# Optimization experiments

Measured on AMD Instinct MI355X. Metric: run time of the kernel, lower is better.

The kernel has to match this reference:

```python
import jax, jax.numpy as jnp
import numpy as np

EPS = 1e-06


def _create_circular_masks(h, w):
    # Faithful to the torch code: y spans width, x spans height -> mask shape (w, h).
    # Only used with square feature maps (h == w), matching the module's implicit assumption.
    cen_w, cen_h = w // 2, h // 2
    y = np.arange(-cen_w, w - cen_w).reshape(-1, 1)
    x = np.arange(-cen_h, h - cen_h).reshape(1, -1)
    y2, x2 = y * y, x * x
    r2 = x2 + y2
    masks = [r2 <= 0]
    max_r = int(np.sqrt(r2.max())) + 1
    quadrants = [(1, 1), (-1, 1), (1, -1), (-1, -1)]  # (sign_x, sign_y)
    for radius in range(1, max_r):
        lo, hi = (radius - 1) ** 2, radius ** 2
        for sx, sy in quadrants:
            quad = (sx * x >= 0) & (sy * y >= 0)
            masks.append((r2 > lo) & (r2 <= hi) & quad)  # ring mask
            masks.append((r2 <= hi) & quad)              # circle mask
    return np.stack(masks).astype(np.float32)  # [M, w, h] == [M, h, w] for square maps


def _l2_normalize(v):
    # v: [B, C]; torch norms over dim=1 with eps added to the norm
    return v / (jnp.linalg.norm(v, axis=1, keepdims=True) + EPS)


def setup_inputs() -> dict:
    key = jax.random.key(0)
    x = jax.random.normal(key, (32, 1024, 28, 28), dtype=jnp.float32)
    return {"x": x}


def reference(x) -> jnp.ndarray:
    B, C, H, W = x.shape
    masks = jnp.asarray(_create_circular_masks(H, W))  # [M, H, W] static constant
    # Global descriptor: max-pool over full map, then channel-wise L2 normalize.
    v = _l2_normalize(jnp.max(x, axis=(2, 3)))  # [B, C]
    # Accumulate masked-max descriptors; scan over the (fixed) mask set keeps
    # peak memory at one masked feature map instead of M of them.
    def step(acc, mask):
        vt = jnp.max(x * mask, axis=(2, 3))  # masked max-pool (zeros included, as in torch)
        return acc + _l2_normalize(vt), None
    v, _ = jax.lax.scan(step, v, masks)
    return v[:, :, None, None]  # [B, C, 1, 1] to match F.max_pool2d output shape
```

## Files before the change

kernel.cpp:

```cpp
#include <hip/hip_runtime.h>
#include <math.h>

#define B_DIM 32
#define C_DIM 1024
#define MAP 784
#define NMASK 153
#define NTERM 154
#define NROW 160
#define NBIN 77
#define DUMMY_BIN 77
#define MAX1 28
#define MAX2 6
#define MPW 8
#define NBLK 1024
#define GRP 32

struct Sched {
    unsigned short off1[MAX1][64];
    unsigned short off2[MAX2][64];
    unsigned char  binA[64];
    unsigned char  binB[64];
    bool ok;
};

constexpr Sched build_sched() {
    Sched S{};
    S.ok = true;
    short px[NBIN][40] = {};
    int   n[NBIN] = {};
    for (int i = 0; i < 28; ++i)
        for (int j = 0; j < 28; ++j) {
            int dy = i - 14, dx = j - 14, r2 = dx * dx + dy * dy;
            int p = i * 28 + j;
            if (r2 == 0) { px[0][n[0]++] = (short)p; continue; }
            if (r2 > 361) continue;
            int r = 0; while (r * r < r2) ++r;
            const int sx[4] = {1, -1, 1, -1}, sy[4] = {1, 1, -1, -1};
            for (int q = 0; q < 4; ++q)
                if (sx[q] * dx >= 0 && sy[q] * dy >= 0) {
                    int b = 1 + q * 19 + (r - 1);
                    if (n[b] >= 40) { S.ok = false; continue; }
                    px[b][n[b]++] = (short)p;
                }
        }
    int ord[NBIN] = {};
    for (int k = 0; k < NBIN; ++k) ord[k] = k;
    for (int a = 0; a < NBIN; ++a) {
        int best = a;
        for (int c = a + 1; c < NBIN; ++c)
            if (n[ord[c]] > n[ord[best]]) best = c;
        int t = ord[a]; ord[a] = ord[best]; ord[best] = t;
    }
    for (int l = 0; l < 64; ++l) {
        S.binA[l] = (unsigned char)ord[l];
        S.binB[l] = (l >= 51) ? (unsigned char)ord[64 + (l - 51)]
                              : (unsigned char)DUMMY_BIN;
        if (n[ord[l]] > MAX1) S.ok = false;
        if (l >= 51 && n[ord[64 + (l - 51)]] > MAX2) S.ok = false;
    }
    {
        bool used[64][40] = {};
        for (int s = 0; s < MAX1; ++s) {
            int bankcnt[32] = {};
            for (int l = 0; l < 64; ++l) {
                int bin = S.binA[l], cnt = n[bin];
                int bestp = 0, bestload = 1 << 30; bool haveUnused = false;
                for (int t = 0; t < cnt; ++t)
                    if (!used[l][t]) {
                        int load = bankcnt[px[bin][t] % 32];
                        if (!haveUnused || load < bestload) { haveUnused = true; bestload = load; bestp = t; }
                    }
                if (!haveUnused)
                    for (int t = 0; t < cnt; ++t) {
                        int load = bankcnt[px[bin][t] % 32];
                        if (load < bestload) { bestload = load; bestp = t; }
                    }
                int p = px[bin][bestp];
                if (haveUnused) used[l][bestp] = true;
                S.off1[s][l] = (unsigned short)(p * 4);
                bankcnt[p % 32]++;
            }
        }
        for (int l = 0; l < 64; ++l)
            for (int t = 0; t < n[S.binA[l]]; ++t)
                if (!used[l][t]) S.ok = false;
    }
    {
        bool used[64][40] = {};
        for (int s = 0; s < MAX2; ++s) {
            int bankcnt[32] = {};
            for (int l = 0; l < 64; ++l) {
                if (S.binB[l] == DUMMY_BIN) {
                    S.off2[s][l] = (unsigned short)((l % 32) * 4);
                    continue;
                }
                int bin = S.binB[l], cnt = n[bin];
                int bestp = 0, bestload = 1 << 30; bool haveUnused = false;
                for (int t = 0; t < cnt; ++t)
                    if (!used[l][t]) {
                        int load = bankcnt[px[bin][t] % 32];
                        if (!haveUnused || load < bestload) { haveUnused = true; bestload = load; bestp = t; }
                    }
                if (!haveUnused)
                    for (int t = 0; t < cnt; ++t) {
                        int load = bankcnt[px[bin][t] % 32];
                        if (load < bestload) { bestload = load; bestp = t; }
                    }
                int p = px[bin][bestp];
                if (haveUnused) used[l][bestp] = true;
                S.off2[s][l] = (unsigned short)(p * 4);
                bankcnt[p % 32]++;
            }
        }
        for (int l = 0; l < 64; ++l)
            if (S.binB[l] != DUMMY_BIN)
                for (int t = 0; t < n[S.binB[l]]; ++t)
                    if (!used[l][t]) S.ok = false;
    }
    return S;
}

static_assert(build_sched().ok, "schedule overflow / unplaced pixel");
__constant__ Sched d_sched = build_sched();

__device__ __forceinline__ int term_addr(int k) {
    if (k == 0) return 0;
    if (k >= NMASK) return DUMMY_BIN;
    int t = k - 1, q = (t >> 1) & 3, rm1 = t >> 3;
    return (t & 1) ? 78 + q * 19 + rm1
                   : 1 + q * 19 + rm1;
}

__global__ __launch_bounds__(256) void cac_fused(const float* __restrict__ x,
                                                 float* __restrict__ partial,
                                                 unsigned int* __restrict__ bar,
                                                 float* __restrict__ out) {
    __shared__ __align__(16) float smap[4][MAP];
    __shared__ float sbuf[4][160];
    __shared__ float ssqred[4][NROW];
    __shared__ float sinv[NROW];

    const int wave = threadIdx.x >> 6;
    const int lane = threadIdx.x & 63;
    const int map0 = blockIdx.x * (4 * MPW) + wave * MPW;

    const int linA = lane % 19;
    const bool inA = lane < 57, inB = lane < 19;
    const int rbA = 1 + lane;
    const int rbB = inB ? 58 + lane : DUMMY_BIN;
    const int a0 = term_addr(lane);
    const int a1 = term_addr(lane + 64);
    const int a2 = term_addr(lane + 128);

    const float4 NEG4 = make_float4(-INFINITY, -INFINITY, -INFINITY, -INFINITY);
    const float4* xp4 = (const float4*)(x + (size_t)map0 * MAP);
    float4 t0 = xp4[lane], t1 = xp4[64 + lane], t2 = xp4[128 + lane];
    float4 t3 = NEG4;
    if (lane < 4) t3 = xp4[192 + lane];

    float* smw = smap[wave];
    float* sbw = sbuf[wave];
    float sq0 = 0.0f, sq1 = 0.0f, sq2 = 0.0f;
    float rr0[MPW], rr1[MPW], rr2[MPW];

    #pragma unroll
    for (int m = 0; m < MPW; ++m) {
        ((float4*)smw)[lane]       = t0;
        ((float4*)smw)[64 + lane]  = t1;
        ((float4*)smw)[128 + lane] = t2;
        if (lane < 4) ((float4*)smw)[192 + lane] = t3;
        float gmax = fmaxf(fmaxf(fmaxf(t0.x, t0.y), fmaxf(t0.z, t0.w)),
                           fmaxf(fmaxf(t1.x, t1.y), fmaxf(t1.z, t1.w)));
        gmax = fmaxf(gmax, fmaxf(fmaxf(t2.x, t2.y), fmaxf(t2.z, t2.w)));
        gmax = fmaxf(gmax, fmaxf(fmaxf(t3.x, t3.y), fmaxf(t3.z, t3.w)));

        if (m < MPW - 1) {
            const float4* np4 = (const float4*)(x + (size_t)(map0 + m + 1) * MAP);
            t0 = np4[lane]; t1 = np4[64 + lane]; t2 = np4[128 + lane];
            t3 = NEG4;
            if (lane < 4) t3 = np4[192 + lane];
        }
        __builtin_amdgcn_wave_barrier();

        const char* base = (const char*)smw;
        float m1 = 0.0f, m2v = 0.0f;
        #pragma unroll
        for (int s = 0; s < MAX1; ++s)
            m1 = fmaxf(m1, *(const float*)(base + d_sched.off1[s][lane]));
        #pragma unroll
        for (int s = 0; s < MAX2; ++s)
            m2v = fmaxf(m2v, *(const float*)(base + d_sched.off2[s][lane]));
        sbw[d_sched.binA[lane]] = m1;
        sbw[d_sched.binB[lane]] = m2v;

        #pragma unroll
        for (int off = 32; off; off >>= 1)
            gmax = fmaxf(gmax, __shfl_xor(gmax, off, 64));
        __builtin_amdgcn_wave_barrier();

        float cval = sbw[0];
        float rA = fmaxf(sbw[rbA], cval);
        float rB = fmaxf(sbw[rbB], cval);
        #pragma unroll
        for (int s = 1; s <= 16; s <<= 1) {
            float uA = __shfl_up(rA, s, 64);
            float uB = __shfl_up(rB, s, 64);
            if (linA >= s) rA = fmaxf(rA, uA);
            if (lane >= s) rB = fmaxf(rB, uB);
        }
        if (inA) sbw[78 + lane] = rA;
        if (inB) sbw[135 + lane] = rB;
        __builtin_amdgcn_wave_barrier();

        float r0 = sbw[a0];
        float r1 = sbw[a1];
        float r2 = sbw[a2];
        r2 = (lane == 25) ? gmax : (lane < 26 ? r2 : 0.0f);

        rr0[m] = r0; rr1[m] = r1; rr2[m] = r2;
        sq0 += r0 * r0; sq1 += r1 * r1; sq2 += r2 * r2;
        __builtin_amdgcn_wave_barrier();
    }

    ssqred[wave][lane]      = sq0;
    ssqred[wave][64 + lane] = sq1;
    if (lane < 32) ssqred[wave][128 + lane] = sq2;
    __syncthreads();
    if (threadIdx.x < NROW) {
        int t = threadIdx.x;
        float v = ssqred[0][t] + ssqred[1][t] + ssqred[2][t] + ssqred[3][t];
        __hip_atomic_store(&partial[(size_t)blockIdx.x * NROW + t], v,
                           __ATOMIC_RELAXED, __HIP_MEMORY_SCOPE_AGENT);
    }
    __syncthreads();

    unsigned int* gbar = bar + (size_t)(blockIdx.x >> 5) * 64;
    if (threadIdx.x == 0) {
        __hip_atomic_fetch_add(gbar, 1u, __ATOMIC_RELAXED, __HIP_MEMORY_SCOPE_AGENT);
        int budget = 1 << 17;
        while (__hip_atomic_load(gbar, __ATOMIC_RELAXED, __HIP_MEMORY_SCOPE_AGENT) < GRP
               && --budget)
            __builtin_amdgcn_s_sleep(16);
    }
    __syncthreads();

    if (threadIdx.x < NROW) {
        int t = threadIdx.x;
        const float* p = partial + (size_t)(blockIdx.x & ~31) * NROW + t;
        float s = 0.0f;
        #pragma unroll 16
        for (int j = 0; j < GRP; ++j)
            s += __hip_atomic_load(&p[(size_t)j * NROW],
                                   __ATOMIC_RELAXED, __HIP_MEMORY_SCOPE_AGENT);
        sinv[t] = (t < NTERM) ? 1.0f / (sqrtf(s) + 1e-6f) : 0.0f;
    }
    __syncthreads();

    const float sl0 = sinv[lane];
    const float sl1 = sinv[64 + lane];
    const float sl2 = (lane < 32) ? sinv[128 + lane] : 0.0f;
    #pragma unroll
    for (int m = 0; m < MPW; ++m) {
        float acc = rr0[m] * sl0 + rr1[m] * sl1 + rr2[m] * sl2;
        #pragma unroll
        for (int off = 32; off; off >>= 1)
            acc += __shfl_xor(acc, off, 64);
        if (lane == 0) out[map0 + m] = acc;
    }
}

extern "C" void kernel_launch(void* const* d_in, const int* in_sizes, int n_in,
                              void* d_out, int out_size, void* d_ws, size_t ws_size,
                              hipStream_t stream) {
    const float* x = (const float*)d_in[0];
    float* out = (float*)d_out;

    float* partial = (float*)d_ws;
    unsigned int* bar = (unsigned int*)((char*)d_ws +
                          (size_t)NBLK * NROW * sizeof(float));

    hipMemsetAsync(bar, 0, 32 * 64 * sizeof(unsigned int), stream);
    cac_fused<<<NBLK, 256, 0, stream>>>(x, partial, bar, out);
}
```

Before: 157.9 us.

## Pair bins across lane pairs to balance per-lane gather work

Bins are now grouped into 32 load-balanced pairs, and each pair's pixels are split evenly over two adjacent lanes. Each lane tracks two partial maxima using per-step select bitmasks, and the pairs are combined with an xor shuffle. This cuts the longest per-lane LDS gather chain from 28 to 18 steps. In exchange each step does extra bitmask tests and selects, and every map adds a shuffle combine.

```diff
diff --git a/kernel.cpp b/kernel.cpp
--- a/kernel.cpp
+++ b/kernel.cpp
@@ -9,7 +9,7 @@
 #define NROW 160
 #define NBIN 77
 #define DUMMY_BIN 77
-#define MAX1 28
+#define MAX1 18
 #define MAX2 6
 #define MPW 8
 #define NBLK 1024
@@ -17,9 +17,11 @@
 
 struct Sched {
     unsigned short off1[MAX1][64];
+    unsigned long long selA[MAX1];
+    unsigned long long selB[MAX1];
     unsigned short off2[MAX2][64];
-    unsigned char  binA[64];
-    unsigned char  binB[64];
+    unsigned char binW[64];
+    unsigned char binB[64];
     bool ok;
 };
 
@@ -52,37 +54,77 @@
         int t = ord[a]; ord[a] = ord[best]; ord[best] = t;
     }
     for (int l = 0; l < 64; ++l) {
-        S.binA[l] = (unsigned char)ord[l];
         S.binB[l] = (l >= 51) ? (unsigned char)ord[64 + (l - 51)]
                               : (unsigned char)DUMMY_BIN;
-        if (n[ord[l]] > MAX1) S.ok = false;
         if (l >= 51 && n[ord[64 + (l - 51)]] > MAX2) S.ok = false;
     }
+
+    int pairBins[32][2] = {};
+    int pairCnt[32] = {};
+    int pairLoad[32] = {};
+    for (int i = 0; i < 64; ++i) {
+        int best = -1;
+        for (int p = 0; p < 32; ++p)
+            if (pairCnt[p] < 2 && (best < 0 || pairLoad[p] < pairLoad[best]))
+                best = p;
+        if (best < 0) { S.ok = false; best = 0; }
+        pairBins[best][pairCnt[best]] = ord[i];
+        pairCnt[best]++;
+        pairLoad[best] += n[ord[i]];
+    }
+
+    short ipix[64][40] = {};
+    signed char iflag[64][40] = {};
+    int icnt[64] = {};
+    for (int p = 0; p < 32; ++p) {
+        int bA = pairBins[p][0], bB = pairBins[p][1];
+        S.binW[2 * p]     = (unsigned char)bA;
+        S.binW[2 * p + 1] = (unsigned char)bB;
+        short cp[80] = {}; signed char cf[80] = {}; int cl = 0;
+        for (int t = 0; t < n[bA]; ++t) { cp[cl] = px[bA][t]; cf[cl] = 0; ++cl; }
+        for (int t = 0; t < n[bB]; ++t) { cp[cl] = px[bB][t]; cf[cl] = 1; ++cl; }
+        int h = (cl + 1) / 2;
+        if (h > MAX1 || (cl - h) > MAX1) S.ok = false;
+        for (int t = 0; t < h && t < 40; ++t) {
+            ipix[2 * p][icnt[2 * p]] = cp[t]; iflag[2 * p][icnt[2 * p]] = cf[t];
+            ++icnt[2 * p];
+        }
+        for (int t = h; t < cl && (t - h) < 40; ++t) {
+            ipix[2 * p + 1][icnt[2 * p + 1]] = cp[t];
+            iflag[2 * p + 1][icnt[2 * p + 1]] = cf[t];
+            ++icnt[2 * p + 1];
+        }
+    }
+
     {
         bool used[64][40] = {};
         for (int s = 0; s < MAX1; ++s) {
             int bankcnt[32] = {};
             for (int l = 0; l < 64; ++l) {
-                int bin = S.binA[l], cnt = n[bin];
+                int cnt = icnt[l];
                 int bestp = 0, bestload = 1 << 30; bool haveUnused = false;
                 for (int t = 0; t < cnt; ++t)
                     if (!used[l][t]) {
-                        int load = bankcnt[px[bin][t] % 32];
+                        int load = bankcnt[ipix[l][t] % 32];
                         if (!haveUnused || load < bestload) { haveUnused = true; bestload = load; bestp = t; }
                     }
                 if (!haveUnused)
                     for (int t = 0; t < cnt; ++t) {
-                        int load = bankcnt[px[bin][t] % 32];
+                        int load = bankcnt[ipix[l][t] % 32];
                         if (load < bestload) { bestload = load; bestp = t; }
                     }
-                int p = px[bin][bestp];
-                if (haveUnused) used[l][bestp] = true;
+                int p = ipix[l][bestp];
                 S.off1[s][l] = (unsigned short)(p * 4);
                 bankcnt[p % 32]++;
+                if (haveUnused) {
+                    used[l][bestp] = true;
+                    if (iflag[l][bestp] == 0) S.selA[s] |= (1ull << l);
+                    else                      S.selB[s] |= (1ull << l);
+                }
             }
         }
         for (int l = 0; l < 64; ++l)
-            for (int t = 0; t < n[S.binA[l]]; ++t)
+            for (int t = 0; t < icnt[l]; ++t)
                 if (!used[l][t]) S.ok = false;
     }
     {
@@ -183,14 +225,21 @@
         __builtin_amdgcn_wave_barrier();
 
         const char* base = (const char*)smw;
-        float m1 = 0.0f, m2v = 0.0f;
-        #pragma unroll
-        for (int s = 0; s < MAX1; ++s)
-            m1 = fmaxf(m1, *(const float*)(base + d_sched.off1[s][lane]));
+        float mAv = 0.0f, mBv = 0.0f, m2v = 0.0f;
+        #pragma unroll
+        for (int s = 0; s < MAX1; ++s) {
+            float v = *(const float*)(base + d_sched.off1[s][lane]);
+            float fa = ((d_sched.selA[s] >> lane) & 1ull) ? v : 0.0f;
+            float fb = ((d_sched.selB[s] >> lane) & 1ull) ? v : 0.0f;
+            mAv = fmaxf(mAv, fa);
+            mBv = fmaxf(mBv, fb);
+        }
         #pragma unroll
         for (int s = 0; s < MAX2; ++s)
             m2v = fmaxf(m2v, *(const float*)(base + d_sched.off2[s][lane]));
-        sbw[d_sched.binA[lane]] = m1;
+        mAv = fmaxf(mAv, __shfl_xor(mAv, 1, 64));
+        mBv = fmaxf(mBv, __shfl_xor(mBv, 1, 64));
+        sbw[d_sched.binW[lane]] = (lane & 1) ? mBv : mAv;
         sbw[d_sched.binB[lane]] = m2v;
 
         #pragma unroll
```

New measurement: 160.4 us. About the same (+1.6%).
